# Kernel optimization log

Hardware: AMD Instinct MI355X
Metric: run time of the kernel (lower is better)

## Reference

```python
import jax, jax.numpy as jnp
import numpy as np

NUM_OPS, B, T, D = 8, 8, 512, 1024


def setup_inputs() -> dict:
    key = jax.random.key(0)
    k1, k2, k3, k4 = jax.random.split(key, 4)
    x = jax.random.normal(k1, (B, T, D), dtype=jnp.float32)
    W = jax.random.normal(k2, (NUM_OPS, D, D), dtype=jnp.float32) * 0.02
    b = jnp.zeros((NUM_OPS, D), dtype=jnp.float32)
    logits = 0.001 * jax.random.normal(k3, (NUM_OPS,), dtype=jnp.float32)
    # uniform noise for Gumbel sampling (matches tf.random.uniform in sample_without_replacement)
    u = jax.random.uniform(k4, (NUM_OPS,), dtype=jnp.float32, minval=1e-6, maxval=1.0 - 1e-6)
    return {"x": x, "W": W, "b": b, "logits": logits, "u": u}


def reference(x, W, b, logits, u):
    # weights = softmax(logits); gumbel top-1 over log(weights) == log_softmax(logits)
    gumbel = -jnp.log(-jnp.log(u))
    idx = jnp.argmax(jax.nn.log_softmax(logits) + gumbel)
    # forward of ops_times_mask_binary: sum over ON ops (num_on_samples=1 -> single op)
    out = jnp.einsum('btd,de->bte', x, W[idx]) + b[idx]  # [B,T,D]
    return out
```

## Files before the change

### kernel.cpp

```cpp
#include <hip/hip_runtime.h>

typedef unsigned short u16;
typedef unsigned int u32;
typedef __attribute__((ext_vector_type(8))) short bf16x8;
typedef __attribute__((ext_vector_type(4))) float f32x4;

#define NUM_OPS 8
#define M_DIM 4096
#define K_DIM 1024
#define N_DIM 1024
#define KITERS 16
#define UNROLL _Pragma("unroll")



__device__ __forceinline__ u16 f2b(float f) {
  union { float f; u32 u; } v; v.f = f;
  u32 r = v.u + 0x7fffu + ((v.u >> 16) & 1u);
  return (u16)(r >> 16);
}

__device__ __forceinline__ u32 pk2(float a, float b) {
  return (u32)f2b(a) | ((u32)f2b(b) << 16);
}

__device__ __forceinline__ int compute_idx(const float* __restrict__ logits,
                                           const float* __restrict__ u) {
  int best = 0; float bv = -3.4e38f;
UNROLL
  for (int i = 0; i < NUM_OPS; ++i) {
    float v = logits[i] - logf(-logf(u[i]));
    if (v > bv) { bv = v; best = i; }
  }
  return best;
}

__global__ void prep_kernel(const float* __restrict__ x, const float* __restrict__ W,
                            const float* __restrict__ logits, const float* __restrict__ u,
                            u16* __restrict__ xb, u16* __restrict__ wt) {
  const int tid = threadIdx.x;
  const int bid = blockIdx.x;
  if (bid < 2048) {
    const int chunk = bid * 4 + (tid >> 6), l = tid & 63;
    const int mtile = chunk >> 5, ktile = chunk & 31;
    const float* src = x + (size_t)(mtile * 16 + (l & 15)) * K_DIM
                         + ktile * 32 + (l >> 4) * 8;
    float4 f0 = *(const float4*)(src);
    float4 f1 = *(const float4*)(src + 4);
    uint4 p;
    p.x = pk2(f0.x, f0.y); p.y = pk2(f0.z, f0.w);
    p.z = pk2(f1.x, f1.y); p.w = pk2(f1.z, f1.w);
    *(uint4*)(xb + (size_t)chunk * 512 + l * 8) = p;
  } else {
    __shared__ u16 t[64][66];
    const int wb = bid - 2048;
    const int kt = wb >> 4, nt = wb & 15;
    const int idx = compute_idx(logits, u);
    const float* Wi = W + (size_t)idx * K_DIM * N_DIM;
UNROLL
    for (int it = 0; it < 16; ++it) {
      int i = it * 256 + tid;
      int r = i >> 6, c = i & 63;
      t[r][c] = f2b(Wi[(size_t)(kt * 64 + r) * N_DIM + nt * 64 + c]);
    }
    __syncthreads();
UNROLL
    for (int it = 0; it < 2; ++it) {
      int s = it * 256 + tid;
      int c = s >> 6, l = s & 63;
      int ntl = c & 3, ktl = c >> 2;
      int kb = ktl * 32 + (l >> 4) * 8, nn = ntl * 16 + (l & 15);
      uint4 p;
      p.x = (u32)t[kb + 0][nn] | ((u32)t[kb + 1][nn] << 16);
      p.y = (u32)t[kb + 2][nn] | ((u32)t[kb + 3][nn] << 16);
      p.z = (u32)t[kb + 4][nn] | ((u32)t[kb + 5][nn] << 16);
      p.w = (u32)t[kb + 6][nn] | ((u32)t[kb + 7][nn] << 16);
      int chunk = (nt * 4 + ntl) * 32 + (kt * 2 + ktl);
      *(uint4*)(wt + (size_t)chunk * 512 + l * 8) = p;
    }
  }
}

__global__ __launch_bounds__(256) void gemm_kernel(
    const u16* __restrict__ xb, const u16* __restrict__ wt,
    const float* __restrict__ bvec, const float* __restrict__ logits,
    const float* __restrict__ u, float* __restrict__ out) {
  const int tid = threadIdx.x;
  const int w = tid >> 6, L = tid & 63;
  const int bid = blockIdx.x;
  const int mb = (bid & 7) * 8 + (bid >> 6);
  const int nb = (bid >> 3) & 7;
  const int wm = w & 1, wn = w >> 1;

  const u16* abase = xb + (size_t)((mb * 4 + 2 * wm) * 32) * 512 + L * 8;
  const u16* bbase = wt + (size_t)((nb * 8 + wn * 4) * 32) * 512 + L * 8;

  f32x4 acc[2][4] = {};
  bf16x8 a0[2][2], b0[4][2], a1[2][2], b1[4][2];

#define LOADF(A, B, kk) do {                                              \
  UNROLL                                                                  \
  for (int f_ = 0; f_ < 2; ++f_)                                          \
    UNROLL                                                                \
    for (int d_ = 0; d_ < 2; ++d_)                                        \
      A[f_][d_] = *(const bf16x8*)(abase + (f_ * 32 + (kk) * 2 + d_) * 512); \
  UNROLL                                                                  \
  for (int t_ = 0; t_ < 4; ++t_)                                          \
    UNROLL                                                                \
    for (int d_ = 0; d_ < 2; ++d_)                                        \
      B[t_][d_] = *(const bf16x8*)(bbase + (t_ * 32 + (kk) * 2 + d_) * 512); \
} while (0)

#define MFMAS(A, B) do {                                                  \
  UNROLL                                                                  \
  for (int d_ = 0; d_ < 2; ++d_)                                          \
    UNROLL                                                                \
    for (int f_ = 0; f_ < 2; ++f_)                                        \
      UNROLL                                                              \
      for (int t_ = 0; t_ < 4; ++t_)                                      \
        acc[f_][t_] = __builtin_amdgcn_mfma_f32_16x16x32_bf16(            \
            A[f_][d_], B[t_][d_], acc[f_][t_], 0, 0, 0);                  \
} while (0)

  LOADF(a0, b0, 0);
  LOADF(a1, b1, 1);

UNROLL
  for (int kk = 0; kk < KITERS; kk += 2) {
    MFMAS(a0, b0);
    if (kk + 2 < KITERS) LOADF(a0, b0, kk + 2);
    MFMAS(a1, b1);
    if (kk + 3 < KITERS) LOADF(a1, b1, kk + 3);
  }

  const int idx = compute_idx(logits, u);
  const float* bi = bvec + (size_t)idx * N_DIM;
UNROLL
  for (int f = 0; f < 2; ++f) {
    int row = mb * 64 + 32 * wm + 16 * f + (L >> 4) * 4;
UNROLL
    for (int t = 0; t < 4; ++t) {
      int col = nb * 128 + 64 * wn + 16 * t + (L & 15);
      float bv = bi[col];
UNROLL
      for (int r = 0; r < 4; ++r)
        out[(size_t)(row + r) * N_DIM + col] = acc[f][t][r] + bv;
    }
  }
}


extern "C" void kernel_launch(void* const* d_in, const int* in_sizes, int n_in,
                              void* d_out, int out_size, void* d_ws, size_t ws_size,
                              hipStream_t stream) {
  const float* x      = (const float*)d_in[0];
  const float* W      = (const float*)d_in[1];
  const float* bvec   = (const float*)d_in[2];
  const float* logits = (const float*)d_in[3];
  const float* u      = (const float*)d_in[4];
  float* out = (float*)d_out;

  u16* xb = (u16*)d_ws;
  u16* wt = (u16*)d_ws + (size_t)M_DIM * K_DIM;

  prep_kernel<<<2048 + 256, 256, 0, stream>>>(x, W, logits, u, xb, wt);
  gemm_kernel<<<512, 256, 0, stream>>>(xb, wt, bvec, logits, u, out);
}
```

Measured before the change: 109.9 us.

## Stage shared B tiles through double-buffered LDS via global_load_lds

```diff
diff --git a/kernel.cpp b/kernel.cpp
--- a/kernel.cpp
+++ b/kernel.cpp
@@ -33,6 +33,13 @@
     if (v > bv) { bv = v; best = i; }
   }
   return best;
+}
+
+__device__ __forceinline__ void gld_lds16(const void* g, void* l) {
+  __builtin_amdgcn_global_load_lds(
+      (__attribute__((address_space(1))) void*)(g),
+      (__attribute__((address_space(3))) void*)(unsigned)(unsigned long long)(l),
+      16, 0, 0);
 }
 
 __global__ void prep_kernel(const float* __restrict__ x, const float* __restrict__ W,
@@ -85,6 +92,8 @@
     const u16* __restrict__ xb, const u16* __restrict__ wt,
     const float* __restrict__ bvec, const float* __restrict__ logits,
     const float* __restrict__ u, float* __restrict__ out) {
+  __shared__ u16 sm[2][16 * 512];
+
   const int tid = threadIdx.x;
   const int w = tid >> 6, L = tid & 63;
   const int bid = blockIdx.x;
@@ -92,26 +101,52 @@
   const int nb = (bid >> 3) & 7;
   const int wm = w & 1, wn = w >> 1;
 
+  const u16* bsrc[4];
+  int blofs[4];
+UNROLL
+  for (int j = 0; j < 4; ++j) {
+    int item = 4 * w + j;
+    int nt = item >> 1, dk = item & 1;
+    bsrc[j] = wt + ((size_t)((nb * 8 + nt) * 32 + dk)) * 512 + L * 8;
+    blofs[j] = item * 512 + L * 8;
+  }
+
+  int boff[4][2];
+UNROLL
+  for (int t = 0; t < 4; ++t)
+UNROLL
+    for (int dk = 0; dk < 2; ++dk)
+      boff[t][dk] = ((4 * wn + t) * 2 + dk) * 512 + L * 8;
+
   const u16* abase = xb + (size_t)((mb * 4 + 2 * wm) * 32) * 512 + L * 8;
-  const u16* bbase = wt + (size_t)((nb * 8 + wn * 4) * 32) * 512 + L * 8;
 
   f32x4 acc[2][4] = {};
-  bf16x8 a0[2][2], b0[4][2], a1[2][2], b1[4][2];
-
-#define LOADF(A, B, kk) do {                                              \
+  bf16x8 aA[2][2], aB[2][2];
+
+#define LOADA(S, k) do {                                                  \
   UNROLL                                                                  \
   for (int f_ = 0; f_ < 2; ++f_)                                          \
     UNROLL                                                                \
     for (int d_ = 0; d_ < 2; ++d_)                                        \
-      A[f_][d_] = *(const bf16x8*)(abase + (f_ * 32 + (kk) * 2 + d_) * 512); \
+      S[f_][d_] = *(const bf16x8*)(abase + (f_ * 32 + (k) * 2 + d_) * 512); \
+} while (0)
+
+#define STAGE_B(k, bufi) do {                                             \
+  const int ko_ = (k) * 1024;        \
+  UNROLL                                                                  \
+  for (int j_ = 0; j_ < 4; ++j_)                                          \
+    gld_lds16(bsrc[j_] + ko_, &sm[bufi][blofs[j_]]);                      \
+} while (0)
+
+#define BODY(S, k, bufi) do {                                             \
+  __syncthreads();   \
+  if ((k) + 1 < KITERS) STAGE_B((k) + 1, (bufi) ^ 1);                     \
+  bf16x8 bf_[4][2];                                                       \
   UNROLL                                                                  \
   for (int t_ = 0; t_ < 4; ++t_)                                          \
     UNROLL                                                                \
     for (int d_ = 0; d_ < 2; ++d_)                                        \
-      B[t_][d_] = *(const bf16x8*)(bbase + (t_ * 32 + (kk) * 2 + d_) * 512); \
-} while (0)
-
-#define MFMAS(A, B) do {                                                  \
+      bf_[t_][d_] = *(const bf16x8*)(&sm[bufi][boff[t_][d_]]);            \
   UNROLL                                                                  \
   for (int d_ = 0; d_ < 2; ++d_)                                          \
     UNROLL                                                                \
@@ -119,18 +154,17 @@
       UNROLL                                                              \
       for (int t_ = 0; t_ < 4; ++t_)                                      \
         acc[f_][t_] = __builtin_amdgcn_mfma_f32_16x16x32_bf16(            \
-            A[f_][d_], B[t_][d_], acc[f_][t_], 0, 0, 0);                  \
+            S[f_][d_], bf_[t_][d_], acc[f_][t_], 0, 0, 0);                \
+  if ((k) + 2 < KITERS) LOADA(S, (k) + 2);   \
 } while (0)
 
-  LOADF(a0, b0, 0);
-  LOADF(a1, b1, 1);
-
-UNROLL
+  LOADA(aA, 0);
+  STAGE_B(0, 0);
+  LOADA(aB, 1);
+
   for (int kk = 0; kk < KITERS; kk += 2) {
-    MFMAS(a0, b0);
-    if (kk + 2 < KITERS) LOADF(a0, b0, kk + 2);
-    MFMAS(a1, b1);
-    if (kk + 3 < KITERS) LOADF(a1, b1, kk + 3);
+    BODY(aA, kk, 0);
+    BODY(aB, kk + 1, 1);
   }
 
   const int idx = compute_idx(logits, u);
```

Result: no change. 107.9 us (-1.8%).
